# Performance work log

Hardware: AMD Instinct MI355X
Metric: run time of the kernel (lower is better)

## Reference

```python
import jax, jax.numpy as jnp
import numpy as np

B, T, E, H, V = 256, 32, 512, 512, 3000
SKIP = 2


def setup_inputs() -> dict:
    key = jax.random.key(0)
    ks = jax.random.split(key, 12)
    # sorted-descending ragged lengths, max forced to T (pack_padded_sequence requires descending)
    lengths = np.sort(np.asarray(jax.random.randint(ks[0], (B,), T // 2, T + 1)))[::-1].copy()
    lengths[0] = T
    s = 0.05
    return {
        "image_features": jax.random.normal(ks[1], (B, E // 2), jnp.float32),
        "text_features": jax.random.normal(ks[2], (B, E // 2), jnp.float32),
        "h0": jnp.zeros((B, H), jnp.float32),
        "c0": jnp.zeros((B, H), jnp.float32),
        "embed_table": jax.random.normal(ks[3], (V, E), jnp.float32) * 0.02,
        "W_ih": jax.random.normal(ks[4], (4 * H, E), jnp.float32) * s,
        "W_hh": jax.random.normal(ks[5], (4 * H, H), jnp.float32) * s,
        "b_ih": jnp.zeros((4 * H,), jnp.float32),
        "b_hh": jnp.zeros((4 * H,), jnp.float32),
        "W_out": jax.random.normal(ks[6], (V, 2 * H), jnp.float32) * s,
        "b_out": jnp.zeros((V,), jnp.float32),
        "answer": jax.random.randint(ks[7], (B, T), 0, V),
        "answer_lengths": lengths,  # numpy int array (static)
    }


def _lstm_cell(x, hx, cx, W_ih, W_hh, b_ih, b_hh):
    # torch.nn.LSTMCell math: gates ordered i, f, g, o
    g = x @ W_ih.T + b_ih + hx @ W_hh.T + b_hh
    i, f, gg, o = jnp.split(g, 4, axis=-1)
    cy = jax.nn.sigmoid(f) * cx + jax.nn.sigmoid(i) * jnp.tanh(gg)
    hy = jax.nn.sigmoid(o) * jnp.tanh(cy)
    return hy, cy


def _packed_indices(lengths, max_len, batch):
    # torch pack_padded_sequence (batch_first) ordering: for each timestep t,
    # rows 0..batch_sizes[t] of the (descending-sorted) batch, time-major concat.
    lengths = np.asarray(lengths)
    idx = np.concatenate([t * batch + np.arange(int((lengths > t).sum())) for t in range(max_len)])
    return jnp.asarray(idx)


def reference(image_features, text_features, h0, c0, embed_table,
              W_ih, W_hh, b_ih, b_hh, W_out, b_out, answer, answer_lengths):
    batch = image_features.shape[0]
    max_len = int(np.max(np.asarray(answer_lengths)))
    combined = jnp.concatenate([image_features, text_features], axis=1)  # [B, E]
    emb = embed_table[answer]                                            # [B, T, E]
    # inputs over time: step 0 = combined, steps 1..max_len-1 = embedded answer tokens
    xs = jnp.concatenate([combined[:, None, :], emb[:, : max_len - 1, :]], axis=1)
    xs = jnp.transpose(xs, (1, 0, 2))                                    # [T, B, E]
    ts = jnp.arange(max_len)

    def step(carry, inp):
        hx, cx, h_m2, h_m1, c_m2, c_m1 = carry
        t, x = inp
        hy, cy = _lstm_cell(x, hx, cx, W_ih, W_hh, b_ih, b_hh)
        # periodic skip-state residual: applied to the carried state AFTER storing hy/cy
        cond = (t >= SKIP) & (t % (SKIP + 1) == 0)
        hx_n = jnp.where(cond, hy + h_m2, hy)
        cx_n = jnp.where(cond, cy + c_m2, cy)
        return (hx_n, cx_n, h_m1, hy, c_m1, cy), (hy, cy)

    z = jnp.zeros_like(h0)
    (_, _, _, _, _, _), (hs, cs) = jax.lax.scan(step, (h0, c0, z, z, z, z), (ts, xs))
    results = jnp.concatenate([hs, cs], axis=-1)          # [T, B, 2H], time-major
    flat = results.reshape(max_len * batch, 2 * results.shape[-1] // 2)
    idx = _packed_indices(answer_lengths, max_len, batch)
    packed = flat[idx]                                    # [sum(lengths), 2H]
    return packed @ W_out.T + b_out                       # [sum(lengths), V]
```

## Files before the change

kernel.cpp:

```cpp
#include <hip/hip_runtime.h>
#include <hip/hip_bf16.h>

#define T_STEPS 32
#define BATCH 256
#define EDIM 512
#define HDIM 512
#define G4 2048
#define VOCAB 3000
#define VPAD 3072

typedef short bf16x8 __attribute__((ext_vector_type(8)));
typedef float f32x4 __attribute__((ext_vector_type(4)));

__device__ __forceinline__ unsigned short f2b(float f){
  union { float f; unsigned int u; } x; x.f = f;
  unsigned int u = x.u;
  unsigned int r = (u + 0x7fffu + ((u >> 16) & 1u)) >> 16;
  return (unsigned short)r;
}
__device__ __forceinline__ float b2f(unsigned short h){
  union { unsigned int u; float f; } x; x.u = ((unsigned int)h) << 16;
  return x.f;
}
__device__ __forceinline__ float sigm(float x){ return 1.0f / (1.0f + expf(-x)); }

__device__ __forceinline__ void gload_lds16(const unsigned short* g, unsigned short* l){
  __builtin_amdgcn_global_load_lds(
      (const __attribute__((address_space(1))) unsigned int*)g,
      (__attribute__((address_space(3))) unsigned int*)l, 16, 0, 0);
}


__global__ void k_cvt_w(const float* __restrict__ wih, const float* __restrict__ whh,
                        unsigned short* __restrict__ o_ih, unsigned short* __restrict__ o_hh){
  int i = blockIdx.x * blockDim.x + threadIdx.x;
  int n1 = G4 * EDIM;
  if (i < n1) o_ih[i] = f2b(wih[i]);
  else { int j = i - n1; if (j < G4 * HDIM) o_hh[j] = f2b(whh[j]); }
}

__global__ void k_cvt_wout(const float* __restrict__ in, unsigned short* __restrict__ out){
  int i = blockIdx.x * blockDim.x + threadIdx.x;
  if (i >= VPAD * 1024) return;
  int r = i >> 10, c = i & 1023;
  float v = (r < VOCAB) ? in[r * 1024 + c] : 0.0f;
  out[i] = f2b(v);
}

__global__ void k_build_xs(const float* __restrict__ img, const float* __restrict__ txt,
                           const float* __restrict__ emb, const int* __restrict__ ans,
                           unsigned short* __restrict__ xs){
  int i = blockIdx.x * blockDim.x + threadIdx.x;
  if (i >= T_STEPS * BATCH * EDIM) return;
  int e = i & (EDIM - 1);
  int r = i >> 9;
  int t = r >> 8, b = r & 255;
  float v;
  if (t == 0) v = (e < 256) ? img[b * 256 + e] : txt[b * 256 + (e - 256)];
  else { int tok = ans[b * T_STEPS + (t - 1)]; v = emb[(size_t)tok * EDIM + e]; }
  xs[i] = f2b(v);
}

__global__ void k_init_carry(const float* __restrict__ h0, const float* __restrict__ c0,
                             unsigned short* __restrict__ hx, float* __restrict__ cx){
  int i = blockIdx.x * blockDim.x + threadIdx.x;
  if (i < BATCH * HDIM){ hx[i] = f2b(h0[i]); cx[i] = c0[i]; }
}

__global__ void k_lens(const int* __restrict__ lengths, int* __restrict__ bs,
                       int* __restrict__ roff, int* __restrict__ meta,
                       int* __restrict__ rmap){
  __shared__ int s[T_STEPS];
  __shared__ int sroff[T_STEPS + 1];
  int t = threadIdx.x;
  if (t < T_STEPS){
    int c = 0;
    for (int i = 0; i < BATCH; i++) c += (lengths[i] > t) ? 1 : 0;
    s[t] = c; bs[t] = c;
  }
  __syncthreads();
  if (t == 0){
    int acc = 0;
    for (int u = 0; u < T_STEPS; u++){ sroff[u] = acc; roff[u] = acc; acc += s[u]; }
    sroff[T_STEPS] = acc;
    meta[0] = acc;
  }
  __syncthreads();
  int ntot = sroff[T_STEPS];
  for (int r = t; r < T_STEPS * BATCH; r += 64){
    int tt = r >> 8, b = r & 255;
    if (b < s[tt]) rmap[sroff[tt] + b] = r;
  }
  for (int r = ntot + t; r < T_STEPS * BATCH; r += 64) rmap[r] = -1;
}

template<int K>
__device__ __forceinline__ void gemm_tile(const unsigned short* __restrict__ A,
                                          const unsigned short* __restrict__ B,
                                          int row0, int col0,
                                          unsigned short* As, unsigned short* Bs,
                                          f32x4 acc[4][4]){
  const int tid = threadIdx.x, w = tid >> 6, l = tid & 63;
  const int la = l & 15, lkq = l >> 4;
  const int sr = l >> 3;
  const int ss = (l & 7) ^ sr;
  const int wr = (w >> 1) * 64, wc = (w & 1) * 64;
  const unsigned short* gA = A + (size_t)(row0 + w * 32 + sr) * K + ss * 8;
  const unsigned short* gB = B + (size_t)(col0 + w * 32 + sr) * K + ss * 8;
  unsigned short* lA = As + (w * 32) * 64;
  unsigned short* lB = Bs + (w * 32) * 64;
  for (int k0 = 0; k0 < K; k0 += 64){
#pragma unroll
    for (int i = 0; i < 4; i++){
      gload_lds16(gA + (size_t)i * 8 * K + k0, lA + i * 8 * 64);
      gload_lds16(gB + (size_t)i * 8 * K + k0, lB + i * 8 * 64);
    }
    __syncthreads();
#pragma unroll
    for (int kk = 0; kk < 2; kk++){
      bf16x8 a[4], b[4];
#pragma unroll
      for (int i = 0; i < 4; i++){
        int r = wr + i * 16 + la;
        a[i] = *(const bf16x8*)(As + r * 64 + (((kk * 4 + lkq) ^ (r & 7)) << 3));
      }
#pragma unroll
      for (int i = 0; i < 4; i++){
        int r = wc + i * 16 + la;
        b[i] = *(const bf16x8*)(Bs + r * 64 + (((kk * 4 + lkq) ^ (r & 7)) << 3));
      }
#pragma unroll
      for (int mi = 0; mi < 4; mi++)
#pragma unroll
        for (int ni = 0; ni < 4; ni++)
          acc[mi][ni] = __builtin_amdgcn_mfma_f32_16x16x32_bf16(a[mi], b[ni], acc[mi][ni], 0, 0, 0);
    }
    __syncthreads();
  }
}

__global__ __launch_bounds__(256) void k_gemm_xw(const unsigned short* __restrict__ A,
                                                 const unsigned short* __restrict__ W,
                                                 const float* __restrict__ bih,
                                                 const float* __restrict__ bhh,
                                                 unsigned short* __restrict__ C){
  __shared__ unsigned short As[128 * 64], Bs[128 * 64];
  int bid = blockIdx.x;
  int xcd = bid & 7, idx = bid >> 3;
  int by = xcd * 2 + (idx & 1);
  int bx = idx >> 1;
  int row0 = bx * 128, col0 = by * 128;
  f32x4 acc[4][4] = {};
  gemm_tile<EDIM>(A, W, row0, col0, As, Bs, acc);
  int tid = threadIdx.x, w = tid >> 6, l = tid & 63;
  int la = l & 15, r4 = (l >> 4) * 4;
  int wr = (w >> 1) * 64, wc = (w & 1) * 64;
#pragma unroll
  for (int ni = 0; ni < 4; ni++){
    int col = col0 + wc + ni * 16 + la;
    float bias = bih[col] + bhh[col];
#pragma unroll
    for (int mi = 0; mi < 4; mi++)
#pragma unroll
      for (int j = 0; j < 4; j++){
        int row = row0 + wr + mi * 16 + r4 + j;
        C[(size_t)row * G4 + col] = f2b(acc[mi][ni][j] + bias);
      }
  }
}

__global__ __launch_bounds__(256, 2) void k_lstm_step(
    const unsigned short* __restrict__ XWt,
    const unsigned short* __restrict__ Whh,
    const unsigned short* __restrict__ hin,
    unsigned short* __restrict__ hout,
    float* __restrict__ cxio,
    unsigned short* __restrict__ hs_t,
    unsigned short* __restrict__ cs_t,
    const unsigned short* __restrict__ hs_m2,
    const unsigned short* __restrict__ cs_m2,
    int do_res){
  __shared__ unsigned short hA[16 * 512];
  __shared__ float gbuf[4][16][17];
  const int w = threadIdx.x >> 6, l = threadIdx.x & 63;
  const int la = l & 15, lkq = l >> 4;
  const int row0 = blockIdx.x * 16;
  const int hc0  = blockIdx.y * 16;
#pragma unroll
  for (int i = 0; i < 4; i++){
    int r = i * 4 + w;
    gload_lds16(hin + (size_t)(row0 + r) * HDIM + ((l ^ (r & 7)) << 3), hA + r * 512);
  }
  const unsigned short* Bp = Whh + (size_t)(w * HDIM + hc0 + la) * HDIM + lkq * 8;
  bf16x8 b[16];
#pragma unroll
  for (int kk = 0; kk < 16; kk++) b[kk] = *(const bf16x8*)(Bp + kk * 32);
  const int r4 = lkq * 4;
  float x[4];
#pragma unroll
  for (int j = 0; j < 4; j++)
    x[j] = b2f(XWt[(size_t)(row0 + r4 + j) * G4 + w * HDIM + hc0 + la]);
  __syncthreads();
  f32x4 acc = {};
#pragma unroll
  for (int kk = 0; kk < 16; kk++){
    bf16x8 a = *(const bf16x8*)(hA + la * 512 + (((kk * 4 + lkq) ^ (la & 7)) << 3));
    acc = __builtin_amdgcn_mfma_f32_16x16x32_bf16(a, b[kk], acc, 0, 0, 0);
  }
#pragma unroll
  for (int j = 0; j < 4; j++) gbuf[w][r4 + j][la] = acc[j] + x[j];
  __syncthreads();
  {
    int r = threadIdx.x >> 4, c = threadIdx.x & 15;
    size_t p = (size_t)(row0 + r) * HDIM + hc0 + c;
    float gi = gbuf[0][r][c], gf = gbuf[1][r][c], gg = gbuf[2][r][c], go = gbuf[3][r][c];
    float cprev = cxio[p];
    float cy = sigm(gf) * cprev + sigm(gi) * tanhf(gg);
    float hy = sigm(go) * tanhf(cy);
    hs_t[p] = f2b(hy);
    cs_t[p] = f2b(cy);
    float hn = hy, cn = cy;
    if (do_res){ hn += b2f(hs_m2[p]); cn += b2f(cs_m2[p]); }
    hout[p] = f2b(hn);
    cxio[p] = cn;
  }
}

__global__ __launch_bounds__(256) void k_gemm_out(const unsigned short* __restrict__ hs,
                                                  const unsigned short* __restrict__ cs,
                                                  const unsigned short* __restrict__ Wo,
                                                  const float* __restrict__ bout,
                                                  const int* __restrict__ meta,
                                                  const int* __restrict__ rmap,
                                                  float* __restrict__ out){
  int ntot = meta[0];
  int bid = blockIdx.x;
  int xcd = bid & 7, idx = bid >> 3;
  int by = xcd * 3 + (idx % 3);
  int bx = idx / 3;
  int row0 = bx * 128, col0 = by * 128;
  if (row0 >= ntot) return;
  __shared__ unsigned short As[128 * 64], Bs[128 * 64];
  const int tid = threadIdx.x, w = tid >> 6, l = tid & 63;
  const int la = l & 15, lkq = l >> 4;
  const int sr = l >> 3, ss = (l & 7) ^ sr;
  const int wr = (w >> 1) * 64, wc = (w & 1) * 64;
  int srow[4];
#pragma unroll
  for (int i = 0; i < 4; i++){
    int rr = rmap[row0 + w * 32 + sr + i * 8];
    srow[i] = rr < 0 ? 0 : rr;
  }
  const unsigned short* gB = Wo + (size_t)(col0 + w * 32 + sr) * 1024 + ss * 8;
  unsigned short* lA = As + (w * 32) * 64;
  unsigned short* lB = Bs + (w * 32) * 64;
  f32x4 acc[4][4] = {};
  for (int k0 = 0; k0 < 1024; k0 += 64){
#pragma unroll
    for (int i = 0; i < 4; i++){
      const unsigned short* srcA = (k0 < 512)
          ? hs + (size_t)srow[i] * 512 + k0 + ss * 8
          : cs + (size_t)srow[i] * 512 + (k0 - 512) + ss * 8;
      gload_lds16(srcA, lA + i * 8 * 64);
      gload_lds16(gB + (size_t)i * 8 * 1024 + k0, lB + i * 8 * 64);
    }
    __syncthreads();
#pragma unroll
    for (int kk = 0; kk < 2; kk++){
      bf16x8 a[4], b[4];
#pragma unroll
      for (int i = 0; i < 4; i++){
        int r = wr + i * 16 + la;
        a[i] = *(const bf16x8*)(As + r * 64 + (((kk * 4 + lkq) ^ (r & 7)) << 3));
      }
#pragma unroll
      for (int i = 0; i < 4; i++){
        int r = wc + i * 16 + la;
        b[i] = *(const bf16x8*)(Bs + r * 64 + (((kk * 4 + lkq) ^ (r & 7)) << 3));
      }
#pragma unroll
      for (int mi = 0; mi < 4; mi++)
#pragma unroll
        for (int ni = 0; ni < 4; ni++)
          acc[mi][ni] = __builtin_amdgcn_mfma_f32_16x16x32_bf16(a[mi], b[ni], acc[mi][ni], 0, 0, 0);
    }
    __syncthreads();
  }
  int r4 = (l >> 4) * 4;
#pragma unroll
  for (int ni = 0; ni < 4; ni++){
    int col = col0 + wc + ni * 16 + la;
    if (col >= VOCAB) continue;
    float bias = bout[col];
#pragma unroll
    for (int mi = 0; mi < 4; mi++)
#pragma unroll
      for (int j = 0; j < 4; j++){
        int row = row0 + wr + mi * 16 + r4 + j;
        if (row < ntot) out[(size_t)row * VOCAB + col] = acc[mi][ni][j] + bias;
      }
  }
}

extern "C" void kernel_launch(void* const* d_in, const int* in_sizes, int n_in,
                              void* d_out, int out_size, void* d_ws, size_t ws_size,
                              hipStream_t stream){
  const float* img   = (const float*)d_in[0];
  const float* txt   = (const float*)d_in[1];
  const float* h0    = (const float*)d_in[2];
  const float* c0    = (const float*)d_in[3];
  const float* emb   = (const float*)d_in[4];
  const float* W_ih  = (const float*)d_in[5];
  const float* W_hh  = (const float*)d_in[6];
  const float* b_ih  = (const float*)d_in[7];
  const float* b_hh  = (const float*)d_in[8];
  const float* W_out = (const float*)d_in[9];
  const float* b_out = (const float*)d_in[10];
  const int* answer  = (const int*)d_in[11];
  const int* lengths = (const int*)d_in[12];
  float* out = (float*)d_out;

  char* ws = (char*)d_ws;
  size_t off = 0;
  auto alloc = [&](size_t bytes) -> void* {
    void* p = ws + off; off += (bytes + 255) & ~(size_t)255; return p;
  };
  unsigned short* Wih_b = (unsigned short*)alloc((size_t)G4 * EDIM * 2);
  unsigned short* Whh_b = (unsigned short*)alloc((size_t)G4 * HDIM * 2);
  unsigned short* Wo_b  = (unsigned short*)alloc((size_t)VPAD * 1024 * 2);
  unsigned short* xs    = (unsigned short*)alloc((size_t)T_STEPS * BATCH * EDIM * 2);
  unsigned short* XW    = (unsigned short*)alloc((size_t)T_STEPS * BATCH * G4 * 2);
  unsigned short* hs    = (unsigned short*)alloc((size_t)T_STEPS * BATCH * HDIM * 2);
  unsigned short* cs    = (unsigned short*)alloc((size_t)T_STEPS * BATCH * HDIM * 2);
  unsigned short* hxA   = (unsigned short*)alloc((size_t)BATCH * HDIM * 2);
  unsigned short* hxB   = (unsigned short*)alloc((size_t)BATCH * HDIM * 2);
  float* cx             = (float*)alloc((size_t)BATCH * HDIM * 4);
  int* bsz  = (int*)alloc(T_STEPS * 4);
  int* roff = (int*)alloc(T_STEPS * 4);
  int* meta = (int*)alloc(256);
  int* rmap = (int*)alloc(T_STEPS * BATCH * 4);

  k_cvt_w<<<(2 * G4 * EDIM + 255) / 256, 256, 0, stream>>>(W_ih, W_hh, Wih_b, Whh_b);
  k_cvt_wout<<<(VPAD * 1024 + 255) / 256, 256, 0, stream>>>(W_out, Wo_b);
  k_build_xs<<<(T_STEPS * BATCH * EDIM + 255) / 256, 256, 0, stream>>>(img, txt, emb, answer, xs);
  k_init_carry<<<(BATCH * HDIM + 255) / 256, 256, 0, stream>>>(h0, c0, hxA, cx);
  k_lens<<<1, 64, 0, stream>>>(lengths, bsz, roff, meta, rmap);

  k_gemm_xw<<<dim3(1024), 256, 0, stream>>>(xs, Wih_b, b_ih, b_hh, XW);

  unsigned short* hbuf[2] = { hxA, hxB };
  for (int t = 0; t < T_STEPS; t++){
    int do_res = (t >= 2 && (t % 3) == 0) ? 1 : 0;
    int tm2 = (t >= 2) ? (t - 2) : 0;
    k_lstm_step<<<dim3(BATCH / 16, HDIM / 16), 256, 0, stream>>>(
        XW + (size_t)t * BATCH * G4, Whh_b, hbuf[t & 1], hbuf[(t + 1) & 1], cx,
        hs + (size_t)t * BATCH * HDIM, cs + (size_t)t * BATCH * HDIM,
        hs + (size_t)tm2 * BATCH * HDIM, cs + (size_t)tm2 * BATCH * HDIM, do_res);
  }

  k_gemm_out<<<dim3(1536), 256, 0, stream>>>(hs, cs, Wo_b, b_out, meta, rmap, out);
}
```

Baseline: 354.5 us.

## Triple-buffer output GEMM with 256x128 tiles, 8 waves, and interleaved staging

Rewrites the final vocabulary projection GEMM to use 512-thread blocks with 256x128 output tiles. LDS tiles are triple-buffered and global-to-LDS loads are issued two k-steps ahead, with explicit vmcnt waits, sched barriers, and priority bumps around the MFMA bursts. This is meant to hide global load latency and raise MFMA utilization in the output projection. In exchange it drops the XCD-aware block swizzle, uses much more LDS per block (which can lower occupancy), and depends on hand-tuned wait counts being correct.

```diff
diff --git a/kernel.cpp b/kernel.cpp
--- a/kernel.cpp
+++ b/kernel.cpp
@@ -29,6 +29,8 @@
       (const __attribute__((address_space(1))) unsigned int*)g,
       (__attribute__((address_space(3))) unsigned int*)l, 16, 0, 0);
 }
+
+#define SB0 __builtin_amdgcn_sched_barrier(0)
 
 
 __global__ void k_cvt_w(const float* __restrict__ wih, const float* __restrict__ whh,
@@ -226,78 +228,121 @@
   }
 }
 
-__global__ __launch_bounds__(256) void k_gemm_out(const unsigned short* __restrict__ hs,
+__global__ __launch_bounds__(512) void k_gemm_out(const unsigned short* __restrict__ hs,
                                                   const unsigned short* __restrict__ cs,
                                                   const unsigned short* __restrict__ Wo,
                                                   const float* __restrict__ bout,
                                                   const int* __restrict__ meta,
                                                   const int* __restrict__ rmap,
                                                   float* __restrict__ out){
-  int ntot = meta[0];
-  int bid = blockIdx.x;
-  int xcd = bid & 7, idx = bid >> 3;
-  int by = xcd * 3 + (idx % 3);
-  int bx = idx / 3;
-  int row0 = bx * 128, col0 = by * 128;
+  const int ntot = meta[0];
+  const int row0 = blockIdx.x * 256, col0 = blockIdx.y * 128;
   if (row0 >= ntot) return;
-  __shared__ unsigned short As[128 * 64], Bs[128 * 64];
-  const int tid = threadIdx.x, w = tid >> 6, l = tid & 63;
+  __shared__ unsigned short As[3][256 * 64];
+  __shared__ unsigned short Bs[3][128 * 64];
+  const int t = threadIdx.x, w = t >> 6, l = t & 63;
   const int la = l & 15, lkq = l >> 4;
-  const int sr = l >> 3, ss = (l & 7) ^ sr;
-  const int wr = (w >> 1) * 64, wc = (w & 1) * 64;
-  int srow[4];
-#pragma unroll
-  for (int i = 0; i < 4; i++){
-    int rr = rmap[row0 + w * 32 + sr + i * 8];
-    srow[i] = rr < 0 ? 0 : rr;
-  }
-  const unsigned short* gB = Wo + (size_t)(col0 + w * 32 + sr) * 1024 + ss * 8;
-  unsigned short* lA = As + (w * 32) * 64;
-  unsigned short* lB = Bs + (w * 32) * 64;
-  f32x4 acc[4][4] = {};
-  for (int k0 = 0; k0 < 1024; k0 += 64){
-#pragma unroll
-    for (int i = 0; i < 4; i++){
-      const unsigned short* srcA = (k0 < 512)
-          ? hs + (size_t)srow[i] * 512 + k0 + ss * 8
-          : cs + (size_t)srow[i] * 512 + (k0 - 512) + ss * 8;
-      gload_lds16(srcA, lA + i * 8 * 64);
-      gload_lds16(gB + (size_t)i * 8 * 1024 + k0, lB + i * 8 * 64);
+  const int wm = w >> 2, wn = w & 3;
+  const int tr = t >> 3, ss = (t & 7) ^ (tr & 7);
+  int srowA[4];
+#pragma unroll
+  for (int p = 0; p < 4; p++){
+    int rr = rmap[row0 + p * 64 + tr];
+    srowA[p] = rr < 0 ? 0 : rr;
+  }
+  f32x4 acc[8][2] = {};
+
+#define STG_A(KT2, P) gload_lds16(                                              \
+    ((KT2) < 8 ? hs : cs) + (size_t)srowA[P] * 512 + ((KT2) & 7) * 64 + ss * 8, \
+    &As[(KT2) % 3][((P) * 64 + w * 8) * 64])
+#define STG_B(KT2, Q) gload_lds16(                                              \
+    Wo + (size_t)(col0 + (Q) * 64 + tr) * 1024 + (KT2) * 64 + ss * 8,           \
+    &Bs[(KT2) % 3][((Q) * 64 + w * 8) * 64])
+
+  STG_A(0,0); STG_A(0,1); STG_A(0,2); STG_A(0,3); STG_B(0,0); STG_B(0,1);
+  STG_A(1,0); STG_A(1,1); STG_A(1,2); STG_A(1,3); STG_B(1,0); STG_B(1,1);
+  SB0;
+  asm volatile("s_waitcnt vmcnt(6)" ::: "memory");
+  SB0; __builtin_amdgcn_s_barrier(); SB0;
+
+  for (int kt = 0; kt < 16; ++kt){
+    const unsigned short* Acur = As[kt % 3];
+    const unsigned short* Bcur = Bs[kt % 3];
+    const int kt2 = kt + 2;
+    const bool st = (kt2 < 16);
+    bf16x8 b[2][2];
+    {
+#pragma unroll
+      for (int nf = 0; nf < 2; nf++){
+        int rc = wn * 32 + nf * 16 + la;
+#pragma unroll
+        for (int kk = 0; kk < 2; kk++)
+          b[nf][kk] = *(const bf16x8*)(Bcur + rc * 64 + (((kk * 4 + lkq) ^ (rc & 7)) << 3));
+      }
+      bf16x8 a[4][2];
+#pragma unroll
+      for (int m2 = 0; m2 < 4; m2++){
+        int rr = wm * 128 + m2 * 16 + la;
+#pragma unroll
+        for (int kk = 0; kk < 2; kk++)
+          a[m2][kk] = *(const bf16x8*)(Acur + rr * 64 + (((kk * 4 + lkq) ^ (rr & 7)) << 3));
+      }
+      if (st){ STG_A(kt2,0); STG_A(kt2,1); STG_B(kt2,0); }
+      SB0; __builtin_amdgcn_s_barrier();
+      asm volatile("s_waitcnt lgkmcnt(0)" ::: "memory");
+      SB0;
+      __builtin_amdgcn_s_setprio(1);
+#pragma unroll
+      for (int m2 = 0; m2 < 4; m2++)
+#pragma unroll
+        for (int nf = 0; nf < 2; nf++)
+#pragma unroll
+          for (int kk = 0; kk < 2; kk++)
+            acc[m2][nf] = __builtin_amdgcn_mfma_f32_16x16x32_bf16(a[m2][kk], b[nf][kk], acc[m2][nf], 0, 0, 0);
+      __builtin_amdgcn_s_setprio(0);
+      SB0; __builtin_amdgcn_s_barrier(); SB0;
     }
-    __syncthreads();
-#pragma unroll
-    for (int kk = 0; kk < 2; kk++){
-      bf16x8 a[4], b[4];
-#pragma unroll
-      for (int i = 0; i < 4; i++){
-        int r = wr + i * 16 + la;
-        a[i] = *(const bf16x8*)(As + r * 64 + (((kk * 4 + lkq) ^ (r & 7)) << 3));
-      }
-#pragma unroll
-      for (int i = 0; i < 4; i++){
-        int r = wc + i * 16 + la;
-        b[i] = *(const bf16x8*)(Bs + r * 64 + (((kk * 4 + lkq) ^ (r & 7)) << 3));
-      }
-#pragma unroll
-      for (int mi = 0; mi < 4; mi++)
-#pragma unroll
-        for (int ni = 0; ni < 4; ni++)
-          acc[mi][ni] = __builtin_amdgcn_mfma_f32_16x16x32_bf16(a[mi], b[ni], acc[mi][ni], 0, 0, 0);
+    {
+      bf16x8 a[4][2];
+#pragma unroll
+      for (int m2 = 0; m2 < 4; m2++){
+        int rr = wm * 128 + (4 + m2) * 16 + la;
+#pragma unroll
+        for (int kk = 0; kk < 2; kk++)
+          a[m2][kk] = *(const bf16x8*)(Acur + rr * 64 + (((kk * 4 + lkq) ^ (rr & 7)) << 3));
+      }
+      if (st){ STG_A(kt2,2); STG_A(kt2,3); STG_B(kt2,1); }
+      SB0; __builtin_amdgcn_s_barrier();
+      asm volatile("s_waitcnt lgkmcnt(0)" ::: "memory");
+      SB0;
+      __builtin_amdgcn_s_setprio(1);
+#pragma unroll
+      for (int m2 = 0; m2 < 4; m2++)
+#pragma unroll
+        for (int nf = 0; nf < 2; nf++)
+#pragma unroll
+          for (int kk = 0; kk < 2; kk++)
+            acc[4 + m2][nf] = __builtin_amdgcn_mfma_f32_16x16x32_bf16(a[m2][kk], b[nf][kk], acc[4 + m2][nf], 0, 0, 0);
+      __builtin_amdgcn_s_setprio(0);
+      SB0;
+      if (kt <= 13){ asm volatile("s_waitcnt vmcnt(6)" ::: "memory"); }
+      else if (kt == 14){ asm volatile("s_waitcnt vmcnt(0)" ::: "memory"); }
+      SB0; __builtin_amdgcn_s_barrier(); SB0;
     }
-    __syncthreads();
-  }
-  int r4 = (l >> 4) * 4;
-#pragma unroll
-  for (int ni = 0; ni < 4; ni++){
-    int col = col0 + wc + ni * 16 + la;
+  }
+#undef STG_A
+#undef STG_B
+#pragma unroll
+  for (int nf = 0; nf < 2; nf++){
+    int col = col0 + wn * 32 + nf * 16 + la;
     if (col >= VOCAB) continue;
     float bias = bout[col];
 #pragma unroll
-    for (int mi = 0; mi < 4; mi++)
+    for (int mf = 0; mf < 8; mf++)
 #pragma unroll
       for (int j = 0; j < 4; j++){
-        int row = row0 + wr + mi * 16 + r4 + j;
-        if (row < ntot) out[(size_t)row * VOCAB + col] = acc[mi][ni][j] + bias;
+        int row = row0 + wm * 128 + mf * 16 + lkq * 4 + j;
+        if (row < ntot) out[(size_t)row * VOCAB + col] = acc[mf][nf][j] + bias;
       }
   }
 }
@@ -358,5 +403,5 @@
         hs + (size_t)tm2 * BATCH * HDIM, cs + (size_t)tm2 * BATCH * HDIM, do_res);
   }
 
-  k_gemm_out<<<dim3(1536), 256, 0, stream>>>(hs, cs, Wo_b, b_out, meta, rmap, out);
-}
+  k_gemm_out<<<dim3(T_STEPS * BATCH / 256, VPAD / 128), 512, 0, stream>>>(hs, cs, Wo_b, b_out, meta, rmap, out);
+}
```

Result: no change. 353.0 us (-0.4%).

## Overlap output projection of previous timestep with each LSTM step in a fused kernel

Applied to the files above, without the earlier changes.

Removes the final large output GEMM and instead fuses a per-timestep output projection (for step t-1) into the LSTM step kernel. Extra blocks compute the output rows for the previous timestep while the remaining blocks run the recurrent step, so the serial recurrence hides the projection work. The projection uses double-buffered LDS staging with explicit waitcnt and barriers, and packed row offsets replace the row map. The cost is a 64KB shared allocation on every block, which may lower occupancy of the step blocks, one extra launch, and only 48 projection blocks per step.

```diff
diff --git a/kernel.cpp b/kernel.cpp
--- a/kernel.cpp
+++ b/kernel.cpp
@@ -8,6 +8,7 @@
 #define G4 2048
 #define VOCAB 3000
 #define VPAD 3072
+#define NOUT_BLK 48
 
 typedef short bf16x8 __attribute__((ext_vector_type(8)));
 typedef float f32x4 __attribute__((ext_vector_type(4)));
@@ -29,6 +30,8 @@
       (const __attribute__((address_space(1))) unsigned int*)g,
       (__attribute__((address_space(3))) unsigned int*)l, 16, 0, 0);
 }
+
+#define SB0 __builtin_amdgcn_sched_barrier(0)
 
 
 __global__ void k_cvt_w(const float* __restrict__ wih, const float* __restrict__ whh,
@@ -68,10 +71,8 @@
 }
 
 __global__ void k_lens(const int* __restrict__ lengths, int* __restrict__ bs,
-                       int* __restrict__ roff, int* __restrict__ meta,
-                       int* __restrict__ rmap){
+                       int* __restrict__ roff, int* __restrict__ meta){
   __shared__ int s[T_STEPS];
-  __shared__ int sroff[T_STEPS + 1];
   int t = threadIdx.x;
   if (t < T_STEPS){
     int c = 0;
@@ -81,17 +82,9 @@
   __syncthreads();
   if (t == 0){
     int acc = 0;
-    for (int u = 0; u < T_STEPS; u++){ sroff[u] = acc; roff[u] = acc; acc += s[u]; }
-    sroff[T_STEPS] = acc;
+    for (int u = 0; u < T_STEPS; u++){ roff[u] = acc; acc += s[u]; }
     meta[0] = acc;
   }
-  __syncthreads();
-  int ntot = sroff[T_STEPS];
-  for (int r = t; r < T_STEPS * BATCH; r += 64){
-    int tt = r >> 8, b = r & 255;
-    if (b < s[tt]) rmap[sroff[tt] + b] = r;
-  }
-  for (int r = ntot + t; r < T_STEPS * BATCH; r += 64) rmap[r] = -1;
 }
 
 template<int K>
@@ -169,23 +162,124 @@
   }
 }
 
-__global__ __launch_bounds__(256, 2) void k_lstm_step(
-    const unsigned short* __restrict__ XWt,
+__global__ __launch_bounds__(256, 2) void k_step_fused(
+    int t,
+    const unsigned short* __restrict__ XW,
     const unsigned short* __restrict__ Whh,
-    const unsigned short* __restrict__ hin,
-    unsigned short* __restrict__ hout,
+    unsigned short* __restrict__ hbA,
+    unsigned short* __restrict__ hbB,
     float* __restrict__ cxio,
-    unsigned short* __restrict__ hs_t,
-    unsigned short* __restrict__ cs_t,
-    const unsigned short* __restrict__ hs_m2,
-    const unsigned short* __restrict__ cs_m2,
-    int do_res){
-  __shared__ unsigned short hA[16 * 512];
-  __shared__ float gbuf[4][16][17];
-  const int w = threadIdx.x >> 6, l = threadIdx.x & 63;
+    unsigned short* __restrict__ hs,
+    unsigned short* __restrict__ cs,
+    const int* __restrict__ bs,
+    const int* __restrict__ roff,
+    const unsigned short* __restrict__ Wo,
+    const float* __restrict__ bout,
+    float* __restrict__ out){
+  __shared__ unsigned char smem[65536];
+  const int bid = blockIdx.x;
+  const int tid = threadIdx.x, w = tid >> 6, l = tid & 63;
   const int la = l & 15, lkq = l >> 4;
-  const int row0 = blockIdx.x * 16;
-  const int hc0  = blockIdx.y * 16;
+
+  if (bid < NOUT_BLK){
+    const int tt = t - 1;
+    if (tt < 0) return;
+    const int rows_t = bs[tt];
+    const int ort = bid & 1, ocp = bid >> 1;
+    const int lrow0 = ort * 128;
+    if (lrow0 >= rows_t) return;
+    const int col0 = ocp * 128;
+    const int orow0 = roff[tt] + lrow0;
+    const unsigned short* Ah = hs + ((size_t)tt * BATCH + lrow0) * 512;
+    const unsigned short* Ac = cs + ((size_t)tt * BATCH + lrow0) * 512;
+    unsigned short* lAs = (unsigned short*)smem;
+    unsigned short* lBs = (unsigned short*)(smem + 32768);
+    const int sr = l >> 3, ss = (l & 7) ^ sr;
+    const int wr = (w >> 1) * 64, wc = (w & 1) * 64;
+    const unsigned short* gB = Wo + (size_t)(col0 + w * 32 + sr) * 1024 + ss * 8;
+    f32x4 acc[4][4] = {};
+
+#define STG_O(BUF, K0)                                                            \
+  { _Pragma("unroll")                                                             \
+    for (int i = 0; i < 4; i++){                                                  \
+      const unsigned short* srcA = ((K0) < 512)                                   \
+          ? Ah + (size_t)(w * 32 + sr + i * 8) * 512 + (K0) + ss * 8              \
+          : Ac + (size_t)(w * 32 + sr + i * 8) * 512 + ((K0) - 512) + ss * 8;     \
+      gload_lds16(srcA, lAs + (BUF) * 8192 + (w * 32 + i * 8) * 64);              \
+      gload_lds16(gB + (size_t)i * 8 * 1024 + (K0), lBs + (BUF) * 8192 + (w * 32 + i * 8) * 64); \
+    } }
+
+    STG_O(0, 0);
+    asm volatile("s_waitcnt vmcnt(0)" ::: "memory"); SB0;
+    __builtin_amdgcn_s_barrier(); SB0;
+    for (int kt = 0; kt < 16; ++kt){
+      int cur = kt & 1;
+      if (kt + 1 < 16){
+        STG_O(cur ^ 1, (kt + 1) * 64); SB0;
+        asm volatile("s_waitcnt vmcnt(8)" ::: "memory");
+      } else {
+        asm volatile("s_waitcnt vmcnt(0)" ::: "memory");
+      }
+      SB0; __builtin_amdgcn_s_barrier(); SB0;
+      const unsigned short* As = lAs + cur * 8192;
+      const unsigned short* Bs = lBs + cur * 8192;
+#pragma unroll
+      for (int kk = 0; kk < 2; kk++){
+        bf16x8 a[4], b[4];
+#pragma unroll
+        for (int i = 0; i < 4; i++){
+          int r = wr + i * 16 + la;
+          a[i] = *(const bf16x8*)(As + r * 64 + (((kk * 4 + lkq) ^ (r & 7)) << 3));
+        }
+#pragma unroll
+        for (int i = 0; i < 4; i++){
+          int r = wc + i * 16 + la;
+          b[i] = *(const bf16x8*)(Bs + r * 64 + (((kk * 4 + lkq) ^ (r & 7)) << 3));
+        }
+#pragma unroll
+        for (int mi = 0; mi < 4; mi++)
+#pragma unroll
+          for (int ni = 0; ni < 4; ni++)
+            acc[mi][ni] = __builtin_amdgcn_mfma_f32_16x16x32_bf16(a[mi], b[ni], acc[mi][ni], 0, 0, 0);
+      }
+      SB0; __builtin_amdgcn_s_barrier(); SB0;
+    }
+#undef STG_O
+    const int nvalid = rows_t - lrow0;
+    int r4 = lkq * 4;
+#pragma unroll
+    for (int ni = 0; ni < 4; ni++){
+      int col = col0 + wc + ni * 16 + la;
+      if (col >= VOCAB) continue;
+      float bias = bout[col];
+#pragma unroll
+      for (int mi = 0; mi < 4; mi++)
+#pragma unroll
+        for (int j = 0; j < 4; j++){
+          int lr = wr + mi * 16 + r4 + j;
+          if (lr < nvalid) out[(size_t)(orow0 + lr) * VOCAB + col] = acc[mi][ni][j] + bias;
+        }
+    }
+    return;
+  }
+
+  if (t >= T_STEPS) return;
+  const int cbid = bid - NOUT_BLK;
+  const int row0 = (cbid & 15) * 16;
+  const int hc0  = (cbid >> 4) * 16;
+  const unsigned short* XWt = XW + (size_t)t * BATCH * G4;
+  const unsigned short* hin = (t & 1) ? hbB : hbA;
+  unsigned short* hout = (t & 1) ? hbA : hbB;
+  unsigned short* hs_t = hs + (size_t)t * BATCH * HDIM;
+  unsigned short* cs_t = cs + (size_t)t * BATCH * HDIM;
+  const int do_res = (t >= 2 && (t % 3) == 0);
+  const int tm2 = (t >= 2) ? (t - 2) : 0;
+  const unsigned short* hs_m2 = hs + (size_t)tm2 * BATCH * HDIM;
+  const unsigned short* cs_m2 = cs + (size_t)tm2 * BATCH * HDIM;
+
+  unsigned short* hA = (unsigned short*)smem;
+  float (*gbuf)[16][17] = (float(*)[16][17])(smem + 16384);
+
 #pragma unroll
   for (int i = 0; i < 4; i++){
     int r = i * 4 + w;
@@ -211,7 +305,7 @@
   for (int j = 0; j < 4; j++) gbuf[w][r4 + j][la] = acc[j] + x[j];
   __syncthreads();
   {
-    int r = threadIdx.x >> 4, c = threadIdx.x & 15;
+    int r = tid >> 4, c = tid & 15;
     size_t p = (size_t)(row0 + r) * HDIM + hc0 + c;
     float gi = gbuf[0][r][c], gf = gbuf[1][r][c], gg = gbuf[2][r][c], go = gbuf[3][r][c];
     float cprev = cxio[p];
@@ -223,82 +317,6 @@
     if (do_res){ hn += b2f(hs_m2[p]); cn += b2f(cs_m2[p]); }
     hout[p] = f2b(hn);
     cxio[p] = cn;
-  }
-}
-
-__global__ __launch_bounds__(256) void k_gemm_out(const unsigned short* __restrict__ hs,
-                                                  const unsigned short* __restrict__ cs,
-                                                  const unsigned short* __restrict__ Wo,
-                                                  const float* __restrict__ bout,
-                                                  const int* __restrict__ meta,
-                                                  const int* __restrict__ rmap,
-                                                  float* __restrict__ out){
-  int ntot = meta[0];
-  int bid = blockIdx.x;
-  int xcd = bid & 7, idx = bid >> 3;
-  int by = xcd * 3 + (idx % 3);
-  int bx = idx / 3;
-  int row0 = bx * 128, col0 = by * 128;
-  if (row0 >= ntot) return;
-  __shared__ unsigned short As[128 * 64], Bs[128 * 64];
-  const int tid = threadIdx.x, w = tid >> 6, l = tid & 63;
-  const int la = l & 15, lkq = l >> 4;
-  const int sr = l >> 3, ss = (l & 7) ^ sr;
-  const int wr = (w >> 1) * 64, wc = (w & 1) * 64;
-  int srow[4];
-#pragma unroll
-  for (int i = 0; i < 4; i++){
-    int rr = rmap[row0 + w * 32 + sr + i * 8];
-    srow[i] = rr < 0 ? 0 : rr;
-  }
-  const unsigned short* gB = Wo + (size_t)(col0 + w * 32 + sr) * 1024 + ss * 8;
-  unsigned short* lA = As + (w * 32) * 64;
-  unsigned short* lB = Bs + (w * 32) * 64;
-  f32x4 acc[4][4] = {};
-  for (int k0 = 0; k0 < 1024; k0 += 64){
-#pragma unroll
-    for (int i = 0; i < 4; i++){
-      const unsigned short* srcA = (k0 < 512)
-          ? hs + (size_t)srow[i] * 512 + k0 + ss * 8
-          : cs + (size_t)srow[i] * 512 + (k0 - 512) + ss * 8;
-      gload_lds16(srcA, lA + i * 8 * 64);
-      gload_lds16(gB + (size_t)i * 8 * 1024 + k0, lB + i * 8 * 64);
-    }
-    __syncthreads();
-#pragma unroll
-    for (int kk = 0; kk < 2; kk++){
-      bf16x8 a[4], b[4];
-#pragma unroll
-      for (int i = 0; i < 4; i++){
-        int r = wr + i * 16 + la;
-        a[i] = *(const bf16x8*)(As + r * 64 + (((kk * 4 + lkq) ^ (r & 7)) << 3));
-      }
-#pragma unroll
-      for (int i = 0; i < 4; i++){
-        int r = wc + i * 16 + la;
-        b[i] = *(const bf16x8*)(Bs + r * 64 + (((kk * 4 + lkq) ^ (r & 7)) << 3));
-      }
-#pragma unroll
-      for (int mi = 0; mi < 4; mi++)
-#pragma unroll
-        for (int ni = 0; ni < 4; ni++)
-          acc[mi][ni] = __builtin_amdgcn_mfma_f32_16x16x32_bf16(a[mi], b[ni], acc[mi][ni], 0, 0, 0);
-    }
-    __syncthreads();
-  }
-  int r4 = (l >> 4) * 4;
-#pragma unroll
-  for (int ni = 0; ni < 4; ni++){
-    int col = col0 + wc + ni * 16 + la;
-    if (col >= VOCAB) continue;
-    float bias = bout[col];
-#pragma unroll
-    for (int mi = 0; mi < 4; mi++)
-#pragma unroll
-      for (int j = 0; j < 4; j++){
-        int row = row0 + wr + mi * 16 + r4 + j;
-        if (row < ntot) out[(size_t)row * VOCAB + col] = acc[mi][ni][j] + bias;
-      }
   }
 }
 
@@ -338,25 +356,17 @@
   int* bsz  = (int*)alloc(T_STEPS * 4);
   int* roff = (int*)alloc(T_STEPS * 4);
   int* meta = (int*)alloc(256);
-  int* rmap = (int*)alloc(T_STEPS * BATCH * 4);
 
   k_cvt_w<<<(2 * G4 * EDIM + 255) / 256, 256, 0, stream>>>(W_ih, W_hh, Wih_b, Whh_b);
   k_cvt_wout<<<(VPAD * 1024 + 255) / 256, 256, 0, stream>>>(W_out, Wo_b);
   k_build_xs<<<(T_STEPS * BATCH * EDIM + 255) / 256, 256, 0, stream>>>(img, txt, emb, answer, xs);
   k_init_carry<<<(BATCH * HDIM + 255) / 256, 256, 0, stream>>>(h0, c0, hxA, cx);
-  k_lens<<<1, 64, 0, stream>>>(lengths, bsz, roff, meta, rmap);
+  k_lens<<<1, 64, 0, stream>>>(lengths, bsz, roff, meta);
 
   k_gemm_xw<<<dim3(1024), 256, 0, stream>>>(xs, Wih_b, b_ih, b_hh, XW);
 
-  unsigned short* hbuf[2] = { hxA, hxB };
-  for (int t = 0; t < T_STEPS; t++){
-    int do_res = (t >= 2 && (t % 3) == 0) ? 1 : 0;
-    int tm2 = (t >= 2) ? (t - 2) : 0;
-    k_lstm_step<<<dim3(BATCH / 16, HDIM / 16), 256, 0, stream>>>(
-        XW + (size_t)t * BATCH * G4, Whh_b, hbuf[t & 1], hbuf[(t + 1) & 1], cx,
-        hs + (size_t)t * BATCH * HDIM, cs + (size_t)t * BATCH * HDIM,
-        hs + (size_t)tm2 * BATCH * HDIM, cs + (size_t)tm2 * BATCH * HDIM, do_res);
-  }
-
-  k_gemm_out<<<dim3(1536), 256, 0, stream>>>(hs, cs, Wo_b, b_out, meta, rmap, out);
-}
+  for (int t = 0; t <= T_STEPS; t++){
+    k_step_fused<<<dim3(NOUT_BLK + 512), 256, 0, stream>>>(
+        t, XW, Whh_b, hxA, hxB, cx, hs, cs, bsz, roff, Wo_b, b_out, out);
+  }
+}
```

Result: slower. 761.5 us (+114.8%).
